# Performance work log

Measured on AMD Instinct MI355X. Metric: run time of the kernel, lower is better.

Reference implementation:

```python
import jax, jax.numpy as jnp
import numpy as np

B, INP, OUP, FGROUP, H, W = 32, 256, 256, 8, 64, 64
CG = INP // FGROUP  # channels per group in GLGF fc1 layers


def conv3x3(x, w):
    # x: (N,1,H,W), w: (1,1,3,3); stride 1, padding 1 (SAME)
    return jax.lax.conv_general_dilated(
        x, w, window_strides=(1, 1), padding='SAME',
        dimension_numbers=('NCHW', 'OIHW', 'NCHW'))


def setup_inputs() -> dict:
    key = jax.random.key(0)
    ks = jax.random.split(key, 8)
    return {
        'x': jax.random.normal(ks[0], (B, INP, H, W), dtype=jnp.float32),
        # GLGF params (all 1x1 convs, bias=False), stored as dense matrices
        'w1l': jax.random.normal(ks[1], (FGROUP, CG, CG), dtype=jnp.float32) * 0.05,   # wn_fc1_l (groups=fgroup)
        'w1g1': jax.random.normal(ks[2], (FGROUP, CG), dtype=jnp.float32) * 0.05,      # wn_fc1_g1 (inp->fgroup, groups=fgroup)
        'w1g2': jax.random.normal(ks[3], (INP, FGROUP), dtype=jnp.float32) * 0.05,     # wn_fc1_g2 (fgroup->inp dense)
        'w2l': jax.random.normal(ks[4], (INP, OUP), dtype=jnp.float32) * 0.05,         # wn_fc2_l (groups=inp): input ch i -> oup outputs
        'w2g': jax.random.normal(ks[5], (INP,), dtype=jnp.float32) * 0.05,             # wn_fc2_g (inp->1 dense)
        'conv1_w': jax.random.normal(ks[6], (1, 1, 3, 3), dtype=jnp.float32) * 0.1,
        'conv2_w': jax.random.normal(ks[7], (1, 1, 3, 3), dtype=jnp.float32) * 0.1,
    }


def reference(x, w1l, w1g1, w1g2, w2l, w2g, conv1_w, conv2_w):
    b, c, h, w_ = x.shape
    fgroup, cg, _ = w1l.shape
    oup = w2l.shape[1]

    # adaptive_avg_pool2d(x, (1,1)) -> (B, inp) descriptor
    g = x.mean(axis=(2, 3))                                   # (B, inp)
    gg = g.reshape(b, fgroup, cg)

    # GLGF: fc1_l (grouped) + fc1_g2(fc1_g1) (squeeze to fgroup then expand)
    local = jnp.einsum('bgi,goi->bgo', gg, w1l).reshape(b, c)  # (B, inp)
    glob = jnp.einsum('bgi,gi->bg', gg, w1g1) @ w1g2.T         # (B, inp)
    s = jax.nn.sigmoid(local + glob)                           # (B, inp)

    # fc2_l (groups=inp): torch channel order is (input_ch g, out j) -> g*oup + j
    # fc2_g adds a per-sample scalar to every channel
    xw = s[:, :, None] * w2l + (s @ w2g)[:, None, None]        # (B, inp, oup)
    # WA_1Conv reinterprets the flat (oup*inp) channels as (oup, inp)
    Wdyn = xw.reshape(b, oup, c)                               # (B, oup, inp)

    # grouped conv with groups=batch, ksize=1 == per-sample matmul
    y = jnp.einsum('bihw,boi->bohw', x, Wdyn)                  # (B, oup, H, W)

    # channel gating: mean over channels -> conv3x3 -> sigmoid -> conv3x3
    cmap = y.mean(axis=1, keepdims=True)                       # (B, 1, H, W)
    cmap = conv3x3(cmap, conv1_w)
    cmap = jax.nn.sigmoid(cmap)
    cmap = conv3x3(cmap, conv2_w)
    return y * cmap
```

## Files before the change

kernel.cpp:

```cpp
#include <hip/hip_runtime.h>
#include <hip/hip_bf16.h>

typedef float  f32x4  __attribute__((ext_vector_type(4)));
typedef short  bf16x8 __attribute__((ext_vector_type(8)));

__device__ __forceinline__ short f2bf(float f) {
    union { __hip_bfloat16 h; short s; } u;
    u.h = __float2bfloat16(f);
    return u.s;
}

__device__ __forceinline__ void gload_lds16(const void* g, void* l) {
    __builtin_amdgcn_global_load_lds(
        (const __attribute__((address_space(1))) unsigned int*)g,
        (__attribute__((address_space(3))) unsigned int*)l, 16, 0, 0);
}

__global__ __launch_bounds__(256) void transpose_kernel(const float* __restrict__ x,
                                                        short* __restrict__ xt,
                                                        float* __restrict__ gpart,
                                                        float* __restrict__ xsump) {
    const int pchunk = blockIdx.x;
    const int cchunk = blockIdx.y;
    const int c0 = cchunk * 64;
    const int b  = blockIdx.z;
    const int tid = threadIdx.x;
    const int cpair = tid >> 3;
    const int poct  = tid & 7;
    const int p0 = pchunk * 64;

    __shared__ unsigned int tile[64 * 32];
    __shared__ float xred[4 * 64];

    const float* rowA = x + ((size_t)(b * 256 + c0 + 2 * cpair)) * 4096 + p0 + poct * 8;
    const float* rowB = rowA + 4096;
    float av[8], bv[8];
    *reinterpret_cast<float4*>(&av[0]) = *reinterpret_cast<const float4*>(rowA);
    *reinterpret_cast<float4*>(&av[4]) = *reinterpret_cast<const float4*>(rowA + 4);
    *reinterpret_cast<float4*>(&bv[0]) = *reinterpret_cast<const float4*>(rowB);
    *reinterpret_cast<float4*>(&bv[4]) = *reinterpret_cast<const float4*>(rowB + 4);

    float sA = 0.f, sB = 0.f;
    #pragma unroll
    for (int e = 0; e < 8; ++e) { sA += av[e]; sB += bv[e]; }
    sA += __shfl_xor(sA, 1, 64); sA += __shfl_xor(sA, 2, 64); sA += __shfl_xor(sA, 4, 64);
    sB += __shfl_xor(sB, 1, 64); sB += __shfl_xor(sB, 2, 64); sB += __shfl_xor(sB, 4, 64);
    if (poct == 0) {
        gpart[((size_t)(b * 256 + c0 + 2 * cpair)) * 64 + pchunk] = sA;
        gpart[((size_t)(b * 256 + c0 + 2 * cpair + 1)) * 64 + pchunk] = sB;
    }

    float xs[8];
    #pragma unroll
    for (int e = 0; e < 8; ++e) {
        float v = av[e] + bv[e];
        v += __shfl_xor(v, 8, 64);
        v += __shfl_xor(v, 16, 64);
        v += __shfl_xor(v, 32, 64);
        xs[e] = v;
    }
    if ((tid & 56) == 0) {
        int wv = tid >> 6;
        #pragma unroll
        for (int e = 0; e < 8; ++e) xred[wv * 64 + poct * 8 + e] = xs[e];
    }

    const int s = cpair >> 2, w = cpair & 3;
    #pragma unroll
    for (int e = 0; e < 8; ++e) {
        int p = poct * 8 + e;
        unsigned int u = (unsigned int)(unsigned short)f2bf(av[e]) |
                         ((unsigned int)(unsigned short)f2bf(bv[e]) << 16);
        tile[p * 32 + ((s ^ poct) << 2) + w] = u;
    }
    __syncthreads();

    if (tid < 64) {
        float v = xred[tid] + xred[64 + tid] + xred[128 + tid] + xred[192 + tid];
        xsump[((size_t)(cchunk * 32 + b)) * 4096 + p0 + tid] = v;
    }

    const int so = tid & 7;
    #pragma unroll
    for (int h = 0; h < 2; ++h) {
        int p = (tid >> 3) + h * 32;
        int sp = so ^ ((p >> 3) & 7);
        uint4 v = *reinterpret_cast<const uint4*>(&tile[p * 32 + sp * 4]);
        *reinterpret_cast<uint4*>(xt + ((size_t)b * 4096 + p0 + p) * 256 + c0 + so * 8) = v;
    }
}

__global__ __launch_bounds__(256) void prep_kernel(
    const float* __restrict__ gpart, const float* __restrict__ w1l,
    const float* __restrict__ w1g1, const float* __restrict__ w1g2,
    const float* __restrict__ w2l, const float* __restrict__ w2g,
    float* __restrict__ s_out, float* __restrict__ t_out,
    float* __restrict__ vq_out, short* __restrict__ w2l_bf) {
    int b = blockIdx.x;
    int tid = threadIdx.x;
    if (b >= 32) {
        int seg = b - 32;
        const float* src = w2l + seg * 4096;
        short* dst = w2l_bf + seg * 4096;
        #pragma unroll
        for (int it = 0; it < 4; ++it) {
            float4 v = *reinterpret_cast<const float4*>(src + it * 1024 + tid * 4);
            short4 o;
            o.x = f2bf(v.x); o.y = f2bf(v.y); o.z = f2bf(v.z); o.w = f2bf(v.w);
            *reinterpret_cast<short4*>(dst + it * 1024 + tid * 4) = o;
        }
        return;
    }
    __shared__ float gs[256];
    __shared__ float zs[8];
    __shared__ float ss[256];
    __shared__ float red[4];
    {
        const float4* gp = reinterpret_cast<const float4*>(gpart + (size_t)(b * 256 + tid) * 64);
        float acc = 0.f;
        #pragma unroll
        for (int j = 0; j < 16; ++j) { float4 v = gp[j]; acc += v.x + v.y + v.z + v.w; }
        gs[tid] = acc * (1.0f / 4096.0f);
    }
    __syncthreads();
    if (tid < 8) {
        float z = 0.f;
        for (int i = 0; i < 32; ++i) z += gs[tid * 32 + i] * w1g1[tid * 32 + i];
        zs[tid] = z;
    }
    __syncthreads();
    int grp = tid >> 5, o = tid & 31;
    float local = 0.f;
    #pragma unroll 4
    for (int i = 0; i < 32; ++i) local += gs[grp * 32 + i] * w1l[grp * 1024 + o * 32 + i];
    float glob = 0.f;
    #pragma unroll
    for (int gg = 0; gg < 8; ++gg) glob += zs[gg] * w1g2[tid * 8 + gg];
    float sv = 1.0f / (1.0f + expf(-(local + glob)));
    ss[tid] = sv;
    s_out[b * 256 + tid] = sv;
    float tv = sv * w2g[tid];
    #pragma unroll
    for (int off = 32; off; off >>= 1) tv += __shfl_down(tv, off, 64);
    if ((tid & 63) == 0) red[tid >> 6] = tv;
    __syncthreads();
    float tb = red[0] + red[1] + red[2] + red[3];
    if (tid == 0) t_out[b] = tb;
    float v = 0.f;
    for (int o2 = 0; o2 < 256; ++o2) v += ss[o2] * w2l[o2 * 256 + tid];
    vq_out[b * 256 + tid] = v * (1.0f / 256.0f);
}

__global__ __launch_bounds__(256) void cmap0_kernel(const short* __restrict__ xt,
                                                    const float* __restrict__ vq,
                                                    const float* __restrict__ t,
                                                    const float* __restrict__ xsump,
                                                    float* __restrict__ cmap0,
                                                    float* __restrict__ txs) {
    const int b = blockIdx.y;
    const int p = blockIdx.x * 256 + threadIdx.x;
    __shared__ float vs[256];
    vs[threadIdx.x] = vq[b * 256 + threadIdx.x];
    __syncthreads();
    const uint4* row = reinterpret_cast<const uint4*>(xt + ((size_t)b * 4096 + p) * 256);
    float acc = 0.f;
    #pragma unroll 8
    for (int it = 0; it < 32; ++it) {
        uint4 u = row[it];
        const unsigned int* uw = reinterpret_cast<const unsigned int*>(&u);
        #pragma unroll
        for (int j = 0; j < 4; ++j) {
            unsigned int wrd = uw[j];
            union { unsigned int u; float f; } lo, hi;
            lo.u = wrd << 16;
            hi.u = wrd & 0xffff0000u;
            acc += lo.f * vs[it * 8 + 2 * j] + hi.f * vs[it * 8 + 2 * j + 1];
        }
    }
    float xs = 0.f;
    #pragma unroll
    for (int part = 0; part < 4; ++part)
        xs += xsump[((size_t)(part * 32 + b)) * 4096 + p];
    float tb = t[b];
    float tx = tb * xs;
    cmap0[b * 4096 + p] = acc + tx;
    txs[b * 4096 + p] = tx;
}

__global__ __launch_bounds__(256) void convs_kernel(const float* __restrict__ cmap0,
                                                    const float* __restrict__ w9a,
                                                    const float* __restrict__ w9b,
                                                    float* __restrict__ cmap) {
    const int strip = blockIdx.x;
    const int b = blockIdx.y;
    const int tid = threadIdx.x;
    const int r0 = strip * 16;
    const int rlo = (r0 == 0) ? 0 : r0 - 1;
    const int rhi = (r0 + 16 > 63) ? 63 : r0 + 16;
    const int cnt = rhi - rlo + 1;

    __shared__ float mid[18 * 64];
    float wa[9], wb[9];
    #pragma unroll
    for (int i = 0; i < 9; ++i) { wa[i] = w9a[i]; wb[i] = w9b[i]; }
    const float* ib = cmap0 + (size_t)b * 4096;

    for (int idx = tid; idx < cnt * 64; idx += 256) {
        int r = rlo + (idx >> 6), cc = idx & 63;
        float acc = 0.f;
        #pragma unroll
        for (int dy = -1; dy <= 1; ++dy)
            #pragma unroll
            for (int dx = -1; dx <= 1; ++dx) {
                int rr = r + dy, xx = cc + dx;
                if (rr >= 0 && rr < 64 && xx >= 0 && xx < 64)
                    acc += ib[rr * 64 + xx] * wa[(dy + 1) * 3 + (dx + 1)];
            }
        mid[idx] = 1.0f / (1.0f + expf(-acc));
    }
    __syncthreads();
    for (int idx = tid; idx < 1024; idx += 256) {
        int r = r0 + (idx >> 6), cc = idx & 63;
        float acc = 0.f;
        #pragma unroll
        for (int dy = -1; dy <= 1; ++dy)
            #pragma unroll
            for (int dx = -1; dx <= 1; ++dx) {
                int rr = r + dy, xx = cc + dx;
                if (rr >= 0 && rr < 64 && xx >= 0 && xx < 64)
                    acc += mid[(rr - rlo) * 64 + xx] * wb[(dy + 1) * 3 + (dx + 1)];
            }
        cmap[(size_t)b * 4096 + r * 64 + cc] = acc;
    }
}

__global__ __launch_bounds__(512) void gemm_epi_kernel(
    const short* __restrict__ xt, const short* __restrict__ w2l_bf,
    const float* __restrict__ s, const float* __restrict__ txs,
    const float* __restrict__ cmap, float* __restrict__ out) {
    const int b  = blockIdx.z;
    const int p0 = blockIdx.x * 64;
    const int tid  = threadIdx.x;
    const int lane = tid & 63;
    const int w    = tid >> 6;
    const int wm = w >> 1, wn = w & 1;

    __shared__ short Alds[2][256 * 64];
    __shared__ short Xlds[2][64 * 64];

    const int sl   = (lane & 7) ^ (lane >> 3);
    const int lrow = lane >> 3;

    f32x4 acc[4][2] = {};

    auto STAGE = [&](int bi, int ks) {
        #pragma unroll
        for (int j = 0; j < 4; ++j) {
            int chunk = w * 4 + j;
            int row = chunk * 8 + lrow;
            gload_lds16(w2l_bf + (size_t)row * 256 + ks + sl * 8,
                        (char*)(&Alds[bi][0]) + chunk * 1024);
        }
        int prow = w * 8 + lrow;
        gload_lds16(xt + ((size_t)b * 4096 + p0 + prow) * 256 + ks + sl * 8,
                    (char*)(&Xlds[bi][0]) + w * 1024);
    };

    STAGE(0, 0);
    #pragma unroll
    for (int t = 0; t < 4; ++t) {
        const int bi = t & 1;
        if (t < 3) {
            STAGE(bi ^ 1, (t + 1) * 64);
            asm volatile("s_waitcnt vmcnt(5)" ::: "memory");
        } else {
            asm volatile("s_waitcnt vmcnt(0)" ::: "memory");
        }
        __builtin_amdgcn_s_barrier();
        asm volatile("" ::: "memory");
        #pragma unroll
        for (int kk = 0; kk < 2; ++kk) {
            bf16x8 af[4], bfr[2];
            const int ss = kk * 4 + (lane >> 4);
            #pragma unroll
            for (int m = 0; m < 4; ++m) {
                int o = wm * 64 + m * 16 + (lane & 15);
                af[m] = *reinterpret_cast<const bf16x8*>(
                    (char*)(&Alds[bi][0]) + o * 128 + ((ss ^ (lane & 7)) * 16));
            }
            #pragma unroll
            for (int n = 0; n < 2; ++n) {
                int p = wn * 32 + n * 16 + (lane & 15);
                bfr[n] = *reinterpret_cast<const bf16x8*>(
                    (char*)(&Xlds[bi][0]) + p * 128 + ((ss ^ (lane & 7)) * 16));
            }
            #pragma unroll
            for (int m = 0; m < 4; ++m)
                #pragma unroll
                for (int n = 0; n < 2; ++n)
                    acc[m][n] = __builtin_amdgcn_mfma_f32_16x16x32_bf16(af[m], bfr[n], acc[m][n], 0, 0, 0);
        }
        asm volatile("" ::: "memory");
        __builtin_amdgcn_s_barrier();
    }
    #pragma unroll
    for (int n = 0; n < 2; ++n) {
        int p = p0 + wn * 32 + n * 16 + (lane & 15);
        float tx = txs[b * 4096 + p];
        float cm = cmap[b * 4096 + p];
        #pragma unroll
        for (int m = 0; m < 4; ++m) {
            #pragma unroll
            for (int r = 0; r < 4; ++r) {
                int o = wm * 64 + m * 16 + (lane >> 4) * 4 + r;
                float yv = s[b * 256 + o] * acc[m][n][r] + tx;
                out[((size_t)b * 256 + o) * 4096 + p] = yv * cm;
            }
        }
    }
}

extern "C" void kernel_launch(void* const* d_in, const int* in_sizes, int n_in,
                              void* d_out, int out_size, void* d_ws, size_t ws_size,
                              hipStream_t stream) {
    const float* x       = (const float*)d_in[0];
    const float* w1l     = (const float*)d_in[1];
    const float* w1g1    = (const float*)d_in[2];
    const float* w1g2    = (const float*)d_in[3];
    const float* w2l     = (const float*)d_in[4];
    const float* w2g     = (const float*)d_in[5];
    const float* conv1_w = (const float*)d_in[6];
    const float* conv2_w = (const float*)d_in[7];
    float* out = (float*)d_out;

    float* wsf    = (float*)d_ws;
    float* s      = wsf;
    float* t      = wsf + 8192;
    float* vq     = wsf + 8256;
    float* cmap0  = wsf + 16448;
    float* txs    = wsf + 147520;
    float* cmap   = wsf + 278592;
    float* gpart  = wsf + 409664;
    float* xsump  = wsf + 933952;
    short* w2l_bf = (short*)(wsf + 1458240);
    short* xt     = (short*)(wsf + 1491008);

    transpose_kernel<<<dim3(64, 4, 32), 256, 0, stream>>>(x, xt, gpart, xsump);
    prep_kernel<<<48, 256, 0, stream>>>(gpart, w1l, w1g1, w1g2, w2l, w2g, s, t, vq, w2l_bf);
    cmap0_kernel<<<dim3(16, 32), 256, 0, stream>>>(xt, vq, t, xsump, cmap0, txs);
    convs_kernel<<<dim3(4, 32), 256, 0, stream>>>(cmap0, conv1_w, conv2_w, cmap);
    gemm_epi_kernel<<<dim3(64, 1, 32), 512, 0, stream>>>(xt, w2l_bf, s, txs, cmap, out);
}
```

Before: 125.5 us.

## Use nontemporal loads/stores, hoist epilogue loads, and halve conv strip height

The transpose kernel now reads x with nontemporal loads. The GEMM epilogue writes its output with nontemporal stores, and its per-pixel and per-channel scale loads are hoisted ahead of the main loop so their latency overlaps the MMA work. The conv kernel uses 8-row strips instead of 16, doubling its block count for more parallelism at the cost of more halo recomputation. The hoisted values add register pressure to the 512-thread GEMM kernel.

```diff
diff --git a/kernel.cpp b/kernel.cpp
--- a/kernel.cpp
+++ b/kernel.cpp
@@ -14,6 +14,14 @@
     __builtin_amdgcn_global_load_lds(
         (const __attribute__((address_space(1))) unsigned int*)g,
         (__attribute__((address_space(3))) unsigned int*)l, 16, 0, 0);
+}
+
+__device__ __forceinline__ void nt_load8(const float* p, float* dst) {
+    const f32x4* vp = reinterpret_cast<const f32x4*>(p);
+    f32x4 a = __builtin_nontemporal_load(vp);
+    f32x4 b = __builtin_nontemporal_load(vp + 1);
+    *reinterpret_cast<f32x4*>(dst)     = a;
+    *reinterpret_cast<f32x4*>(dst + 4) = b;
 }
 
 __global__ __launch_bounds__(256) void transpose_kernel(const float* __restrict__ x,
@@ -35,10 +43,8 @@
     const float* rowA = x + ((size_t)(b * 256 + c0 + 2 * cpair)) * 4096 + p0 + poct * 8;
     const float* rowB = rowA + 4096;
     float av[8], bv[8];
-    *reinterpret_cast<float4*>(&av[0]) = *reinterpret_cast<const float4*>(rowA);
-    *reinterpret_cast<float4*>(&av[4]) = *reinterpret_cast<const float4*>(rowA + 4);
-    *reinterpret_cast<float4*>(&bv[0]) = *reinterpret_cast<const float4*>(rowB);
-    *reinterpret_cast<float4*>(&bv[4]) = *reinterpret_cast<const float4*>(rowB + 4);
+    nt_load8(rowA, av);
+    nt_load8(rowB, bv);
 
     float sA = 0.f, sB = 0.f;
     #pragma unroll
@@ -194,12 +200,12 @@
     const int strip = blockIdx.x;
     const int b = blockIdx.y;
     const int tid = threadIdx.x;
-    const int r0 = strip * 16;
+    const int r0 = strip * 8;
     const int rlo = (r0 == 0) ? 0 : r0 - 1;
-    const int rhi = (r0 + 16 > 63) ? 63 : r0 + 16;
+    const int rhi = (r0 + 8 > 63) ? 63 : r0 + 8;
     const int cnt = rhi - rlo + 1;
 
-    __shared__ float mid[18 * 64];
+    __shared__ float mid[10 * 64];
     float wa[9], wb[9];
     #pragma unroll
     for (int i = 0; i < 9; ++i) { wa[i] = w9a[i]; wb[i] = w9b[i]; }
@@ -219,7 +225,7 @@
         mid[idx] = 1.0f / (1.0f + expf(-acc));
     }
     __syncthreads();
-    for (int idx = tid; idx < 1024; idx += 256) {
+    for (int idx = tid; idx < 512; idx += 256) {
         int r = r0 + (idx >> 6), cc = idx & 63;
         float acc = 0.f;
         #pragma unroll
@@ -251,6 +257,19 @@
     const int sl   = (lane & 7) ^ (lane >> 3);
     const int lrow = lane >> 3;
 
+    float txr[2], cmr[2], sv[4][4];
+    #pragma unroll
+    for (int n = 0; n < 2; ++n) {
+        int p = p0 + wn * 32 + n * 16 + (lane & 15);
+        txr[n] = txs[b * 4096 + p];
+        cmr[n] = cmap[b * 4096 + p];
+    }
+    #pragma unroll
+    for (int m = 0; m < 4; ++m)
+        #pragma unroll
+        for (int r = 0; r < 4; ++r)
+            sv[m][r] = s[b * 256 + wm * 64 + m * 16 + (lane >> 4) * 4 + r];
+
     f32x4 acc[4][2] = {};
 
     auto STAGE = [&](int bi, int ks) {
@@ -306,15 +325,13 @@
     #pragma unroll
     for (int n = 0; n < 2; ++n) {
         int p = p0 + wn * 32 + n * 16 + (lane & 15);
-        float tx = txs[b * 4096 + p];
-        float cm = cmap[b * 4096 + p];
         #pragma unroll
         for (int m = 0; m < 4; ++m) {
             #pragma unroll
             for (int r = 0; r < 4; ++r) {
                 int o = wm * 64 + m * 16 + (lane >> 4) * 4 + r;
-                float yv = s[b * 256 + o] * acc[m][n][r] + tx;
-                out[((size_t)b * 256 + o) * 4096 + p] = yv * cm;
+                float yv = (sv[m][r] * acc[m][n][r] + txr[n]) * cmr[n];
+                __builtin_nontemporal_store(yv, &out[((size_t)b * 256 + o) * 4096 + p]);
             }
         }
     }
@@ -348,6 +365,6 @@
     transpose_kernel<<<dim3(64, 4, 32), 256, 0, stream>>>(x, xt, gpart, xsump);
     prep_kernel<<<48, 256, 0, stream>>>(gpart, w1l, w1g1, w1g2, w2l, w2g, s, t, vq, w2l_bf);
     cmap0_kernel<<<dim3(16, 32), 256, 0, stream>>>(xt, vq, t, xsump, cmap0, txs);
-    convs_kernel<<<dim3(4, 32), 256, 0, stream>>>(cmap0, conv1_w, conv2_w, cmap);
+    convs_kernel<<<dim3(8, 32), 256, 0, stream>>>(cmap0, conv1_w, conv2_w, cmap);
     gemm_epi_kernel<<<dim3(64, 1, 32), 512, 0, stream>>>(xt, w2l_bf, s, txs, cmap, out);
 }
```

Result: faster. 119.0 us (-5.2%).
